# Kernel optimization log

Measured on AMD Instinct MI355X. Metric: run time of the kernel, lower is better.

## Reference

```python
import jax, jax.numpy as jnp
import numpy as np

B, T, E, H, DK, FF = 8, 2048, 64, 8, 8, 256
EPS = 1e-5


def _ln(x, g, b):
    m = jnp.mean(x, axis=-1, keepdims=True)
    v = jnp.mean((x - m) ** 2, axis=-1, keepdims=True)
    return (x - m) * jax.lax.rsqrt(v + EPS) * g + b


def setup_inputs() -> dict:
    key = jax.random.key(0)
    ks = jax.random.split(key, 16)
    s = 0.05
    f32 = jnp.float32
    return {
        "x": jax.random.normal(ks[0], (B, T, E), f32),
        "Wq": jax.random.normal(ks[1], (E, E), f32) * s,
        "bq": jnp.zeros((E,), f32),
        "Wk": jax.random.normal(ks[2], (E, E), f32) * s,
        "bk": jnp.zeros((E,), f32),
        "Wv": jax.random.normal(ks[3], (E, E), f32) * s,
        "bv": jnp.zeros((E,), f32),
        "Wo": jax.random.normal(ks[4], (E, E), f32) * s,
        "bo": jnp.zeros((E,), f32),
        "theta_attn": jax.random.uniform(ks[5], (), f32, 0.0, 2.0 * np.pi),
        "theta_ffn": jax.random.uniform(ks[6], (), f32, 0.0, 2.0 * np.pi),
        "W1": jax.random.normal(ks[7], (FF, E), f32) * s,
        "b1": jnp.zeros((FF,), f32),
        "W2": jax.random.normal(ks[8], (E, FF), f32) * s,
        "b2": jnp.zeros((E,), f32),
        "g1": jnp.ones((E,), f32),
        "be1": jnp.zeros((E,), f32),
        "g2": jnp.ones((E,), f32),
        "be2": jnp.zeros((E,), f32),
    }


def _forward(x, Wq, bq, Wk, bk, Wv, bv, Wo, bo, theta_attn, theta_ffn,
             W1, b1, W2, b2, g1, be1, g2, be2):
    def split(h):  # [B,T,E] -> [B,H,T,DK]
        return h.reshape(B, T, H, DK).transpose(0, 2, 1, 3)

    q = split(x @ Wq.T + bq)
    k = split(x @ Wk.T + bk)
    v = split(x @ Wv.T + bv)
    # per-head quantum circuit: RX(x) then shared RX(theta) -> <Z> = cos(x + theta)
    q = jnp.cos(q + theta_attn)
    k = jnp.cos(k + theta_attn)
    v = jnp.cos(v + theta_attn)
    scores = jnp.einsum('bhtd,bhsd->bhts', q, k) / np.float32(np.sqrt(DK))
    scores = jax.nn.softmax(scores, axis=-1)
    attn = jnp.einsum('bhts,bhsd->bhtd', scores, v)
    attn = attn.transpose(0, 2, 1, 3).reshape(B, T, E) @ Wo.T + bo
    x1 = _ln(x + attn, g1, be1)
    # FFN quantum circuit: RX(x) then shared RY(theta) -> <Z> = cos(x)*cos(theta)
    qout = jnp.cos(x1) * jnp.cos(theta_ffn)
    f = jax.nn.relu(qout @ W1.T + b1) @ W2.T + b2
    return _ln(x1 + f, g2, be2)


def reference(x, Wq, bq, Wk, bk, Wv, bv, Wo, bo, theta_attn, theta_ffn,
              W1, b1, W2, b2, g1, be1, g2, be2):
    return _forward(x, Wq, bq, Wk, bk, Wv, bv, Wo, bo, theta_attn, theta_ffn,
                    W1, b1, W2, b2, g1, be1, g2, be2)
```

## Files before the change

### kernel.cpp

```cpp
#include <hip/hip_runtime.h>
#include <hip/hip_bf16.h>

#define B_ 8
#define T_ 2048
#define NROWS 16384

typedef __attribute__((ext_vector_type(4))) float f32x4;
typedef __attribute__((ext_vector_type(16))) float f32x16;
typedef __attribute__((ext_vector_type(8))) short short8;
typedef __fp16 half2_t __attribute__((ext_vector_type(2)));

__device__ __forceinline__ unsigned short f2bf(float f) {
    __hip_bfloat16 h = __float2bfloat16(f);
    return *reinterpret_cast<unsigned short*>(&h);
}
__device__ __forceinline__ unsigned int pkrtz(float a, float b) {
    half2_t h = __builtin_amdgcn_cvt_pkrtz(a, b);
    return __builtin_bit_cast(unsigned int, h);
}
__device__ __forceinline__ float dot2(unsigned int a, unsigned int b, float c) {
    return __builtin_amdgcn_fdot2(__builtin_bit_cast(half2_t, a),
                                  __builtin_bit_cast(half2_t, b), c, false);
}
__device__ __forceinline__ float fast_exp2(float x) {
#if __has_builtin(__builtin_amdgcn_exp2f)
    return __builtin_amdgcn_exp2f(x);
#else
    return exp2f(x);
#endif
}

__global__ __launch_bounds__(512, 4) void qkv_kernel(
    const float* __restrict__ x,
    const float* __restrict__ Wq, const float* __restrict__ bq,
    const float* __restrict__ Wk, const float* __restrict__ bk,
    const float* __restrict__ Wv, const float* __restrict__ bv,
    const float* __restrict__ theta_attn,
    unsigned short* __restrict__ qb, unsigned short* __restrict__ kbuf,
    unsigned short* __restrict__ vbuf)
{
    __shared__ unsigned int xpk[32][34];
    __shared__ unsigned int wpk[32][196];
    const int tid = threadIdx.x;
    const int n0 = blockIdx.x * 32;

    {
        float4 v = ((const float4*)(x + (size_t)n0 * 64))[tid];
        int r = tid >> 4, k0 = (tid & 15) * 4;
        xpk[(k0 >> 1) + 0][r] = pkrtz(v.x, v.y);
        xpk[(k0 >> 1) + 1][r] = pkrtz(v.z, v.w);
    }
    const float* Wm[3] = {Wq, Wk, Wv};
    #pragma unroll
    for (int t = 0; t < 6; t++) {
        int fi = tid + t * 512;
        int m = fi >> 10, j = (fi >> 4) & 63, k0 = (fi & 15) * 4;
        float4 v = ((const float4*)Wm[m])[fi & 1023];
        wpk[(k0 >> 1) + 0][m * 64 + j] = pkrtz(v.x, v.y);
        wpk[(k0 >> 1) + 1][m * 64 + j] = pkrtz(v.z, v.w);
    }
    __syncthreads();

    const int r = tid >> 4;
    const int c0 = (tid & 15) * 12;
    float acc[12] = {};
    #pragma unroll 8
    for (int kp = 0; kp < 32; kp++) {
        unsigned int a = xpk[kp][r];
        uint4 b0 = *(const uint4*)&wpk[kp][c0];
        uint4 b1 = *(const uint4*)&wpk[kp][c0 + 4];
        uint4 b2 = *(const uint4*)&wpk[kp][c0 + 8];
        unsigned int bb[12] = {b0.x, b0.y, b0.z, b0.w,
                               b1.x, b1.y, b1.z, b1.w,
                               b2.x, b2.y, b2.z, b2.w};
        #pragma unroll
        for (int j = 0; j < 12; j++) acc[j] = dot2(a, bb[j], acc[j]);
    }

    const float th = *theta_attn;
    const float QS = 0.51006980f;
    const float* biasp[3] = {bq, bk, bv};
    unsigned short* outp3[3] = {qb, kbuf, vbuf};
    const int n = n0 + r;
    const int bI = n >> 11, tI = n & 2047;
    #pragma unroll
    for (int j = 0; j < 12; j++) {
        int c = c0 + j;
        int m = c >> 6, cc = c & 63;
        float val = __cosf(acc[j] + biasp[m][cc] + th);
        if (m == 0) val *= QS;
        size_t idx = ((size_t)(bI * 8 + (cc >> 3)) * 2048 + tI) * 8 + (cc & 7);
        outp3[m][idx] = f2bf(val);
    }
}

__global__ __launch_bounds__(256, 4) void attn_kernel(
    const unsigned short* __restrict__ qb,
    const unsigned short* __restrict__ kbuf,
    const unsigned short* __restrict__ vbuf,
    float* __restrict__ attn)
{
    __shared__ unsigned short Ks[1024 * 8];
    __shared__ unsigned short Vt[8 * 1032];
    const int tid = threadIdx.x;
    const int head = blockIdx.x >> 4;
    const int qblk = blockIdx.x & 15;
    const size_t hoff = (size_t)head * T_ * 8;
    const int wave = tid >> 6, lane = tid & 63;
    const int col = lane & 31, h = lane >> 5;
    const int q0 = qblk * 128 + wave * 32;

    const short8 z8 = {0, 0, 0, 0, 0, 0, 0, 0};
    short8 bqf = z8;
    if (h == 0) bqf = *(const short8*)(qb + hoff + (size_t)(q0 + col) * 8);

    f32x16 oacc = {0.f,0.f,0.f,0.f,0.f,0.f,0.f,0.f,0.f,0.f,0.f,0.f,0.f,0.f,0.f,0.f};
    const f32x16 z16 = {0.f,0.f,0.f,0.f,0.f,0.f,0.f,0.f,0.f,0.f,0.f,0.f,0.f,0.f,0.f,0.f};
    float lsum = 0.f;

    for (int half = 0; half < 2; half++) {
        __syncthreads();
        {
            const uint4* kg = (const uint4*)(kbuf + hoff + (size_t)half * 1024 * 8);
            const uint4* vg = (const uint4*)(vbuf + hoff + (size_t)half * 1024 * 8);
            uint4* kl = (uint4*)Ks;
            #pragma unroll
            for (int it = 0; it < 4; it++) {
                int s = tid + it * 256;
                kl[s] = kg[s];
                union { uint4 u; unsigned short us[8]; } cv;
                cv.u = vg[s];
                #pragma unroll
                for (int d = 0; d < 8; d++) Vt[d * 1032 + s] = cv.us[d];
            }
        }
        __syncthreads();

        for (int s0 = 0; s0 < 1024; s0 += 32) {
            short8 ak = z8;
            if (h == 0) ak = *(const short8*)&Ks[(s0 + col) * 8];
            f32x16 S = __builtin_amdgcn_mfma_f32_32x32x16_bf16(ak, bqf, z16, 0, 0, 0);
            float p[16];
            #pragma unroll
            for (int rr = 0; rr < 16; rr++) {
                p[rr] = fast_exp2(S[rr]);
                lsum += p[rr];
            }
            #pragma unroll
            for (int g = 0; g < 2; g++) {
                const float* pp = p + g * 8;
                unsigned int q01 = __builtin_amdgcn_perm(__float_as_uint(pp[1]), __float_as_uint(pp[0]), 0x07060302u);
                unsigned int q23 = __builtin_amdgcn_perm(__float_as_uint(pp[3]), __float_as_uint(pp[2]), 0x07060302u);
                unsigned int q45 = __builtin_amdgcn_perm(__float_as_uint(pp[5]), __float_as_uint(pp[4]), 0x07060302u);
                unsigned int q67 = __builtin_amdgcn_perm(__float_as_uint(pp[7]), __float_as_uint(pp[6]), 0x07060302u);
                unsigned int x01 = (unsigned int)__shfl_xor((int)q01, 32);
                unsigned int x23 = (unsigned int)__shfl_xor((int)q23, 32);
                unsigned int x45 = (unsigned int)__shfl_xor((int)q45, 32);
                unsigned int x67 = (unsigned int)__shfl_xor((int)q67, 32);
                union { unsigned int u[4]; short8 s; } bp;
                bp.u[0] = h ? x45 : q01;
                bp.u[1] = h ? x67 : q23;
                bp.u[2] = h ? q45 : x01;
                bp.u[3] = h ? q67 : x23;
                short8 av = z8;
                if (col < 8) av = *(const short8*)&Vt[col * 1032 + s0 + g * 16 + 8 * h];
                oacc = __builtin_amdgcn_mfma_f32_32x32x16_bf16(av, bp.s, oacc, 0, 0, 0);
            }
        }
    }

    lsum += __shfl_xor(lsum, 32);
    const float inv = 1.0f / lsum;
    const int bI = head >> 3, hI = head & 7;
    const int q = q0 + col;
    #pragma unroll
    for (int rr = 0; rr < 4; rr++) {
        int d = 4 * h + rr;
        attn[((size_t)bI * 2048 + q) * 64 + hI * 8 + d] = oacc[rr] * inv;
    }
}

__global__ __launch_bounds__(512, 4) void tail_kernel(
    const float* __restrict__ attn, const float* __restrict__ x,
    const float* __restrict__ Wo, const float* __restrict__ bo,
    const float* __restrict__ g1, const float* __restrict__ be1,
    const float* __restrict__ theta_ffn,
    const float* __restrict__ W1, const float* __restrict__ b1,
    const float* __restrict__ W2, const float* __restrict__ b2,
    const float* __restrict__ g2, const float* __restrict__ be2,
    float* __restrict__ outp)
{
    __shared__ unsigned int Wbuf[8704];
    __shared__ unsigned int qpk[32 * 66];
    __shared__ unsigned int Upk[128 * 66];
    const int tid = threadIdx.x;
    const int n0 = blockIdx.x * 64;
    const int r0 = (tid >> 4) * 2;
    const int c0 = (tid & 15) * 4;

    {
        const float4* ag = (const float4*)(attn + (size_t)n0 * 64);
        #pragma unroll
        for (int t = 0; t < 2; t++) {
            int fi = tid + t * 512;
            float4 v = ag[fi];
            int rr = fi >> 4, k0 = (fi & 15) * 4;
            Upk[((k0 >> 1) + 0) * 66 + rr] = pkrtz(v.x, v.y);
            Upk[((k0 >> 1) + 1) * 66 + rr] = pkrtz(v.z, v.w);
        }
        #pragma unroll
        for (int t = 0; t < 2; t++) {
            int fi = tid + t * 512;
            float4 v = ((const float4*)Wo)[fi];
            int nn = fi >> 4, k0 = (fi & 15) * 4;
            Wbuf[((k0 >> 1) + 0) * 68 + nn] = pkrtz(v.x, v.y);
            Wbuf[((k0 >> 1) + 1) * 68 + nn] = pkrtz(v.z, v.w);
        }
    }
    __syncthreads();

    float acc1[2][4] = {};
    #pragma unroll 8
    for (int kp = 0; kp < 32; kp++) {
        unsigned int a0 = Upk[kp * 66 + r0];
        unsigned int a1 = Upk[kp * 66 + r0 + 1];
        uint4 b = *(const uint4*)&Wbuf[kp * 68 + c0];
        unsigned int bb[4] = {b.x, b.y, b.z, b.w};
        #pragma unroll
        for (int j = 0; j < 4; j++) {
            acc1[0][j] = dot2(a0, bb[j], acc1[0][j]);
            acc1[1][j] = dot2(a1, bb[j], acc1[1][j]);
        }
    }

    float x1v[2][4];
    {
        float4 bo4 = *(const float4*)&bo[c0];
        float4 g14 = *(const float4*)&g1[c0];
        float4 be14 = *(const float4*)&be1[c0];
        float gg[4] = {g14.x, g14.y, g14.z, g14.w};
        float eb[4] = {be14.x, be14.y, be14.z, be14.w};
        float bb[4] = {bo4.x, bo4.y, bo4.z, bo4.w};
        float cth = __cosf(*theta_ffn);
        #pragma unroll
        for (int i = 0; i < 2; i++) {
            float4 xv = *(const float4*)(x + (size_t)(n0 + r0 + i) * 64 + c0);
            float vv[4] = {xv.x + acc1[i][0] + bb[0], xv.y + acc1[i][1] + bb[1],
                           xv.z + acc1[i][2] + bb[2], xv.w + acc1[i][3] + bb[3]};
            float s1 = vv[0] + vv[1] + vv[2] + vv[3];
            float s2 = vv[0]*vv[0] + vv[1]*vv[1] + vv[2]*vv[2] + vv[3]*vv[3];
            #pragma unroll
            for (int m = 1; m <= 8; m <<= 1) {
                s1 += __shfl_xor(s1, m, 16);
                s2 += __shfl_xor(s2, m, 16);
            }
            float mean = s1 * 0.015625f;
            float rstd = rsqrtf(s2 * 0.015625f - mean * mean + 1e-5f);
            float qv[4];
            #pragma unroll
            for (int j = 0; j < 4; j++) {
                x1v[i][j] = (vv[j] - mean) * rstd * gg[j] + eb[j];
                qv[j] = __cosf(x1v[i][j]) * cth;
            }
            qpk[((c0 >> 1) + 0) * 66 + r0 + i] = pkrtz(qv[0], qv[1]);
            qpk[((c0 >> 1) + 1) * 66 + r0 + i] = pkrtz(qv[2], qv[3]);
        }
    }
    __syncthreads();

    #pragma unroll
    for (int t = 0; t < 8; t++) {
        int fi = tid + t * 512;
        float4 v = ((const float4*)W1)[fi];
        int f = fi >> 4, k0 = (fi & 15) * 4;
        Wbuf[((k0 >> 1) + 0) * 260 + f] = pkrtz(v.x, v.y);
        Wbuf[((k0 >> 1) + 1) * 260 + f] = pkrtz(v.z, v.w);
    }
    __syncthreads();

    const int r2 = (tid >> 5) * 4;
    const int f0 = (tid & 31) * 8;
    float acc2[4][8] = {};
    #pragma unroll 4
    for (int kp = 0; kp < 32; kp++) {
        unsigned int a_[4];
        #pragma unroll
        for (int i = 0; i < 4; i++) a_[i] = qpk[kp * 66 + r2 + i];
        uint4 b0 = *(const uint4*)&Wbuf[kp * 260 + f0];
        uint4 b1_ = *(const uint4*)&Wbuf[kp * 260 + f0 + 4];
        unsigned int bb[8] = {b0.x, b0.y, b0.z, b0.w, b1_.x, b1_.y, b1_.z, b1_.w};
        #pragma unroll
        for (int i = 0; i < 4; i++)
            #pragma unroll
            for (int j = 0; j < 8; j++)
                acc2[i][j] = dot2(a_[i], bb[j], acc2[i][j]);
    }
    {
        float4 c1a = *(const float4*)&b1[f0];
        float4 c1b = *(const float4*)&b1[f0 + 4];
        float bb[8] = {c1a.x, c1a.y, c1a.z, c1a.w, c1b.x, c1b.y, c1b.z, c1b.w};
        #pragma unroll
        for (int i = 0; i < 4; i++) {
            float hv[8];
            #pragma unroll
            for (int j = 0; j < 8; j++) hv[j] = fmaxf(acc2[i][j] + bb[j], 0.f);
            #pragma unroll
            for (int jp = 0; jp < 4; jp++)
                Upk[(f0 / 2 + jp) * 66 + r2 + i] = pkrtz(hv[2 * jp], hv[2 * jp + 1]);
        }
    }
    __syncthreads();

    #pragma unroll
    for (int t = 0; t < 8; t++) {
        int fi = tid + t * 512;
        float4 v = ((const float4*)W2)[fi];
        int e = fi >> 6, k0 = (fi & 63) * 4;
        Wbuf[((k0 >> 1) + 0) * 68 + e] = pkrtz(v.x, v.y);
        Wbuf[((k0 >> 1) + 1) * 68 + e] = pkrtz(v.z, v.w);
    }
    __syncthreads();

    float acc3[2][4] = {};
    #pragma unroll 8
    for (int fp = 0; fp < 128; fp++) {
        unsigned int a0 = Upk[fp * 66 + r0];
        unsigned int a1 = Upk[fp * 66 + r0 + 1];
        uint4 b = *(const uint4*)&Wbuf[fp * 68 + c0];
        unsigned int bb[4] = {b.x, b.y, b.z, b.w};
        #pragma unroll
        for (int j = 0; j < 4; j++) {
            acc3[0][j] = dot2(a0, bb[j], acc3[0][j]);
            acc3[1][j] = dot2(a1, bb[j], acc3[1][j]);
        }
    }

    {
        float4 b24 = *(const float4*)&b2[c0];
        float4 g24 = *(const float4*)&g2[c0];
        float4 be24 = *(const float4*)&be2[c0];
        float bb[4] = {b24.x, b24.y, b24.z, b24.w};
        float gg[4] = {g24.x, g24.y, g24.z, g24.w};
        float eb[4] = {be24.x, be24.y, be24.z, be24.w};
        #pragma unroll
        for (int i = 0; i < 2; i++) {
            float vv[4];
            #pragma unroll
            for (int j = 0; j < 4; j++) vv[j] = x1v[i][j] + acc3[i][j] + bb[j];
            float s1 = vv[0] + vv[1] + vv[2] + vv[3];
            float s2 = vv[0]*vv[0] + vv[1]*vv[1] + vv[2]*vv[2] + vv[3]*vv[3];
            #pragma unroll
            for (int m = 1; m <= 8; m <<= 1) {
                s1 += __shfl_xor(s1, m, 16);
                s2 += __shfl_xor(s2, m, 16);
            }
            float mean = s1 * 0.015625f;
            float rstd = rsqrtf(s2 * 0.015625f - mean * mean + 1e-5f);
            float4 o;
            o.x = (vv[0] - mean) * rstd * gg[0] + eb[0];
            o.y = (vv[1] - mean) * rstd * gg[1] + eb[1];
            o.z = (vv[2] - mean) * rstd * gg[2] + eb[2];
            o.w = (vv[3] - mean) * rstd * gg[3] + eb[3];
            *(float4*)(outp + (size_t)(n0 + r0 + i) * 64 + c0) = o;
        }
    }
}

extern "C" void kernel_launch(void* const* d_in, const int* in_sizes, int n_in,
                              void* d_out, int out_size, void* d_ws, size_t ws_size,
                              hipStream_t stream)
{
    const float* x   = (const float*)d_in[0];
    const float* Wq  = (const float*)d_in[1];
    const float* bq  = (const float*)d_in[2];
    const float* Wk  = (const float*)d_in[3];
    const float* bk  = (const float*)d_in[4];
    const float* Wv  = (const float*)d_in[5];
    const float* bv  = (const float*)d_in[6];
    const float* Wo  = (const float*)d_in[7];
    const float* bo  = (const float*)d_in[8];
    const float* tha = (const float*)d_in[9];
    const float* thf = (const float*)d_in[10];
    const float* W1  = (const float*)d_in[11];
    const float* b1  = (const float*)d_in[12];
    const float* W2  = (const float*)d_in[13];
    const float* b2  = (const float*)d_in[14];
    const float* g1  = (const float*)d_in[15];
    const float* be1 = (const float*)d_in[16];
    const float* g2  = (const float*)d_in[17];
    const float* be2 = (const float*)d_in[18];

    char* wsb = (char*)d_ws;
    unsigned short* qbp = (unsigned short*)(wsb);
    unsigned short* kbp = (unsigned short*)(wsb + (2u << 20));
    unsigned short* vbp = (unsigned short*)(wsb + (4u << 20));
    float* attn = (float*)(wsb + (6u << 20));

    qkv_kernel<<<512, 512, 0, stream>>>(x, Wq, bq, Wk, bk, Wv, bv, tha, qbp, kbp, vbp);
    attn_kernel<<<1024, 256, 0, stream>>>(qbp, kbp, vbp, attn);
    tail_kernel<<<256, 512, 0, stream>>>(attn, x, Wo, bo, g1, be1, thf,
                                         W1, b1, W2, b2, g2, be2, (float*)d_out);
}
```

Before: 170.6 us.

## Stage QKV output through LDS for vector stores; halve tail tile and prefetch weights

```diff
diff --git a/kernel.cpp b/kernel.cpp
--- a/kernel.cpp
+++ b/kernel.cpp
@@ -41,6 +41,7 @@
 {
     __shared__ unsigned int xpk[32][34];
     __shared__ unsigned int wpk[32][196];
+    __shared__ unsigned short outs[32][216];
     const int tid = threadIdx.x;
     const int n0 = blockIdx.x * 32;
 
@@ -80,17 +81,36 @@
     const float th = *theta_attn;
     const float QS = 0.51006980f;
     const float* biasp[3] = {bq, bk, bv};
+    {
+        float vals[12];
+        #pragma unroll
+        for (int j = 0; j < 12; j++) {
+            int c = c0 + j;
+            int m = c >> 6, cc = c & 63;
+            float v = __cosf(acc[j] + biasp[m][cc] + th);
+            vals[j] = (m == 0) ? v * QS : v;
+        }
+        unsigned int* orow = (unsigned int*)&outs[r][c0];
+        #pragma unroll
+        for (int jp = 0; jp < 6; jp++)
+            orow[jp] = (unsigned int)f2bf(vals[2 * jp]) |
+                       ((unsigned int)f2bf(vals[2 * jp + 1]) << 16);
+    }
+    __syncthreads();
+
     unsigned short* outp3[3] = {qb, kbuf, vbuf};
-    const int n = n0 + r;
-    const int bI = n >> 11, tI = n & 2047;
-    #pragma unroll
-    for (int j = 0; j < 12; j++) {
-        int c = c0 + j;
-        int m = c >> 6, cc = c & 63;
-        float val = __cosf(acc[j] + biasp[m][cc] + th);
-        if (m == 0) val *= QS;
-        size_t idx = ((size_t)(bI * 8 + (cc >> 3)) * 2048 + tI) * 8 + (cc & 7);
-        outp3[m][idx] = f2bf(val);
+    #pragma unroll
+    for (int t = 0; t < 2; t++) {
+        int fi = tid + t * 512;
+        if (fi < 768) {
+            int m = fi >> 8, rest = fi & 255;
+            int hI = rest >> 5, r2 = rest & 31;
+            uint4 v = *(const uint4*)&outs[r2][m * 64 + hI * 8];
+            int n = n0 + r2;
+            unsigned short* dst = outp3[m] +
+                ((size_t)((n >> 11) * 8 + hI) * 2048 + (n & 2047)) * 8;
+            *(uint4*)dst = v;
+        }
     }
 }
 
@@ -190,123 +210,121 @@
     const float* __restrict__ g2, const float* __restrict__ be2,
     float* __restrict__ outp)
 {
-    __shared__ unsigned int Wbuf[8704];
-    __shared__ unsigned int qpk[32 * 66];
-    __shared__ unsigned int Upk[128 * 66];
+    __shared__ unsigned int Wbuf[10880];
+    __shared__ unsigned int qpk[32 * 34];
+    __shared__ unsigned int Upk[128 * 34];
     const int tid = threadIdx.x;
-    const int n0 = blockIdx.x * 64;
-    const int r0 = (tid >> 4) * 2;
+    const int n0 = blockIdx.x * 32;
+    const int r0 = tid >> 4;
     const int c0 = (tid & 15) * 4;
-
-    {
-        const float4* ag = (const float4*)(attn + (size_t)n0 * 64);
-        #pragma unroll
-        for (int t = 0; t < 2; t++) {
-            int fi = tid + t * 512;
-            float4 v = ag[fi];
-            int rr = fi >> 4, k0 = (fi & 15) * 4;
-            Upk[((k0 >> 1) + 0) * 66 + rr] = pkrtz(v.x, v.y);
-            Upk[((k0 >> 1) + 1) * 66 + rr] = pkrtz(v.z, v.w);
-        }
-        #pragma unroll
-        for (int t = 0; t < 2; t++) {
-            int fi = tid + t * 512;
-            float4 v = ((const float4*)Wo)[fi];
-            int nn = fi >> 4, k0 = (fi & 15) * 4;
-            Wbuf[((k0 >> 1) + 0) * 68 + nn] = pkrtz(v.x, v.y);
-            Wbuf[((k0 >> 1) + 1) * 68 + nn] = pkrtz(v.z, v.w);
-        }
-    }
-    __syncthreads();
-
-    float acc1[2][4] = {};
+    unsigned int* const W1p = Wbuf + 2176;
+    unsigned int* const W2p = Wbuf + 2176;
+
+    float4 atv = ((const float4*)(attn + (size_t)n0 * 64))[tid];
+    float4 wo0 = ((const float4*)Wo)[tid];
+    float4 wo1 = ((const float4*)Wo)[tid + 512];
+    float4 xv  = *(const float4*)(x + (size_t)(n0 + r0) * 64 + c0);
+    float4 w1r[8];
+    #pragma unroll
+    for (int t = 0; t < 8; t++) w1r[t] = ((const float4*)W1)[tid + t * 512];
+
+    {
+        int rr = tid >> 4, k0 = (tid & 15) * 4;
+        Upk[((k0 >> 1) + 0) * 34 + rr] = pkrtz(atv.x, atv.y);
+        Upk[((k0 >> 1) + 1) * 34 + rr] = pkrtz(atv.z, atv.w);
+    }
+    {
+        int nn = tid >> 4, k0 = (tid & 15) * 4;
+        Wbuf[((k0 >> 1) + 0) * 68 + nn] = pkrtz(wo0.x, wo0.y);
+        Wbuf[((k0 >> 1) + 1) * 68 + nn] = pkrtz(wo0.z, wo0.w);
+        int fi = tid + 512;
+        nn = fi >> 4; k0 = (fi & 15) * 4;
+        Wbuf[((k0 >> 1) + 0) * 68 + nn] = pkrtz(wo1.x, wo1.y);
+        Wbuf[((k0 >> 1) + 1) * 68 + nn] = pkrtz(wo1.z, wo1.w);
+    }
+    __syncthreads();
+
+    #pragma unroll
+    for (int t = 0; t < 8; t++) {
+        int fi = tid + t * 512;
+        int f = fi >> 4, k0 = (fi & 15) * 4;
+        W1p[((k0 >> 1) + 0) * 260 + f] = pkrtz(w1r[t].x, w1r[t].y);
+        W1p[((k0 >> 1) + 1) * 260 + f] = pkrtz(w1r[t].z, w1r[t].w);
+    }
+
+    float acc1[4] = {};
     #pragma unroll 8
     for (int kp = 0; kp < 32; kp++) {
-        unsigned int a0 = Upk[kp * 66 + r0];
-        unsigned int a1 = Upk[kp * 66 + r0 + 1];
+        unsigned int a = Upk[kp * 34 + r0];
         uint4 b = *(const uint4*)&Wbuf[kp * 68 + c0];
-        unsigned int bb[4] = {b.x, b.y, b.z, b.w};
-        #pragma unroll
-        for (int j = 0; j < 4; j++) {
-            acc1[0][j] = dot2(a0, bb[j], acc1[0][j]);
-            acc1[1][j] = dot2(a1, bb[j], acc1[1][j]);
-        }
-    }
-
-    float x1v[2][4];
+        acc1[0] = dot2(a, b.x, acc1[0]);
+        acc1[1] = dot2(a, b.y, acc1[1]);
+        acc1[2] = dot2(a, b.z, acc1[2]);
+        acc1[3] = dot2(a, b.w, acc1[3]);
+    }
+
+    float x1v[4];
     {
         float4 bo4 = *(const float4*)&bo[c0];
         float4 g14 = *(const float4*)&g1[c0];
         float4 be14 = *(const float4*)&be1[c0];
+        float cth = __cosf(*theta_ffn);
+        float vv[4] = {xv.x + acc1[0] + bo4.x, xv.y + acc1[1] + bo4.y,
+                       xv.z + acc1[2] + bo4.z, xv.w + acc1[3] + bo4.w};
+        float s1 = vv[0] + vv[1] + vv[2] + vv[3];
+        float s2 = vv[0]*vv[0] + vv[1]*vv[1] + vv[2]*vv[2] + vv[3]*vv[3];
+        #pragma unroll
+        for (int m = 1; m <= 8; m <<= 1) {
+            s1 += __shfl_xor(s1, m, 16);
+            s2 += __shfl_xor(s2, m, 16);
+        }
+        float mean = s1 * 0.015625f;
+        float rstd = rsqrtf(s2 * 0.015625f - mean * mean + 1e-5f);
         float gg[4] = {g14.x, g14.y, g14.z, g14.w};
         float eb[4] = {be14.x, be14.y, be14.z, be14.w};
-        float bb[4] = {bo4.x, bo4.y, bo4.z, bo4.w};
-        float cth = __cosf(*theta_ffn);
-        #pragma unroll
-        for (int i = 0; i < 2; i++) {
-            float4 xv = *(const float4*)(x + (size_t)(n0 + r0 + i) * 64 + c0);
-            float vv[4] = {xv.x + acc1[i][0] + bb[0], xv.y + acc1[i][1] + bb[1],
-                           xv.z + acc1[i][2] + bb[2], xv.w + acc1[i][3] + bb[3]};
-            float s1 = vv[0] + vv[1] + vv[2] + vv[3];
-            float s2 = vv[0]*vv[0] + vv[1]*vv[1] + vv[2]*vv[2] + vv[3]*vv[3];
-            #pragma unroll
-            for (int m = 1; m <= 8; m <<= 1) {
-                s1 += __shfl_xor(s1, m, 16);
-                s2 += __shfl_xor(s2, m, 16);
-            }
-            float mean = s1 * 0.015625f;
-            float rstd = rsqrtf(s2 * 0.015625f - mean * mean + 1e-5f);
-            float qv[4];
-            #pragma unroll
-            for (int j = 0; j < 4; j++) {
-                x1v[i][j] = (vv[j] - mean) * rstd * gg[j] + eb[j];
-                qv[j] = __cosf(x1v[i][j]) * cth;
-            }
-            qpk[((c0 >> 1) + 0) * 66 + r0 + i] = pkrtz(qv[0], qv[1]);
-            qpk[((c0 >> 1) + 1) * 66 + r0 + i] = pkrtz(qv[2], qv[3]);
-        }
-    }
-    __syncthreads();
-
-    #pragma unroll
-    for (int t = 0; t < 8; t++) {
-        int fi = tid + t * 512;
-        float4 v = ((const float4*)W1)[fi];
-        int f = fi >> 4, k0 = (fi & 15) * 4;
-        Wbuf[((k0 >> 1) + 0) * 260 + f] = pkrtz(v.x, v.y);
-        Wbuf[((k0 >> 1) + 1) * 260 + f] = pkrtz(v.z, v.w);
-    }
-    __syncthreads();
-
-    const int r2 = (tid >> 5) * 4;
+        float qv[4];
+        #pragma unroll
+        for (int j = 0; j < 4; j++) {
+            x1v[j] = (vv[j] - mean) * rstd * gg[j] + eb[j];
+            qv[j] = __cosf(x1v[j]) * cth;
+        }
+        qpk[((c0 >> 1) + 0) * 34 + r0] = pkrtz(qv[0], qv[1]);
+        qpk[((c0 >> 1) + 1) * 34 + r0] = pkrtz(qv[2], qv[3]);
+    }
+    __syncthreads();
+
+    float4 w2r[8];
+    #pragma unroll
+    for (int t = 0; t < 8; t++) w2r[t] = ((const float4*)W2)[tid + t * 512];
+
+    const int r2 = (tid >> 5) * 2;
     const int f0 = (tid & 31) * 8;
-    float acc2[4][8] = {};
+    float acc2[2][8] = {};
     #pragma unroll 4
     for (int kp = 0; kp < 32; kp++) {
-        unsigned int a_[4];
-        #pragma unroll
-        for (int i = 0; i < 4; i++) a_[i] = qpk[kp * 66 + r2 + i];
-        uint4 b0 = *(const uint4*)&Wbuf[kp * 260 + f0];
-        uint4 b1_ = *(const uint4*)&Wbuf[kp * 260 + f0 + 4];
+        unsigned int a0 = qpk[kp * 34 + r2];
+        unsigned int a1 = qpk[kp * 34 + r2 + 1];
+        uint4 b0 = *(const uint4*)&W1p[kp * 260 + f0];
+        uint4 b1_ = *(const uint4*)&W1p[kp * 260 + f0 + 4];
         unsigned int bb[8] = {b0.x, b0.y, b0.z, b0.w, b1_.x, b1_.y, b1_.z, b1_.w};
         #pragma unroll
-        for (int i = 0; i < 4; i++)
-            #pragma unroll
-            for (int j = 0; j < 8; j++)
-                acc2[i][j] = dot2(a_[i], bb[j], acc2[i][j]);
+        for (int j = 0; j < 8; j++) {
+            acc2[0][j] = dot2(a0, bb[j], acc2[0][j]);
+            acc2[1][j] = dot2(a1, bb[j], acc2[1][j]);
+        }
     }
     {
         float4 c1a = *(const float4*)&b1[f0];
         float4 c1b = *(const float4*)&b1[f0 + 4];
         float bb[8] = {c1a.x, c1a.y, c1a.z, c1a.w, c1b.x, c1b.y, c1b.z, c1b.w};
         #pragma unroll
-        for (int i = 0; i < 4; i++) {
+        for (int i = 0; i < 2; i++) {
             float hv[8];
             #pragma unroll
             for (int j = 0; j < 8; j++) hv[j] = fmaxf(acc2[i][j] + bb[j], 0.f);
             #pragma unroll
             for (int jp = 0; jp < 4; jp++)
-                Upk[(f0 / 2 + jp) * 66 + r2 + i] = pkrtz(hv[2 * jp], hv[2 * jp + 1]);
+                Upk[(f0 / 2 + jp) * 34 + r2 + i] = pkrtz(hv[2 * jp], hv[2 * jp + 1]);
         }
     }
     __syncthreads();
@@ -314,55 +332,44 @@
     #pragma unroll
     for (int t = 0; t < 8; t++) {
         int fi = tid + t * 512;
-        float4 v = ((const float4*)W2)[fi];
         int e = fi >> 6, k0 = (fi & 63) * 4;
-        Wbuf[((k0 >> 1) + 0) * 68 + e] = pkrtz(v.x, v.y);
-        Wbuf[((k0 >> 1) + 1) * 68 + e] = pkrtz(v.z, v.w);
-    }
-    __syncthreads();
-
-    float acc3[2][4] = {};
+        W2p[((k0 >> 1) + 0) * 68 + e] = pkrtz(w2r[t].x, w2r[t].y);
+        W2p[((k0 >> 1) + 1) * 68 + e] = pkrtz(w2r[t].z, w2r[t].w);
+    }
+    __syncthreads();
+
+    float acc3[4] = {};
     #pragma unroll 8
     for (int fp = 0; fp < 128; fp++) {
-        unsigned int a0 = Upk[fp * 66 + r0];
-        unsigned int a1 = Upk[fp * 66 + r0 + 1];
-        uint4 b = *(const uint4*)&Wbuf[fp * 68 + c0];
-        unsigned int bb[4] = {b.x, b.y, b.z, b.w};
-        #pragma unroll
-        for (int j = 0; j < 4; j++) {
-            acc3[0][j] = dot2(a0, bb[j], acc3[0][j]);
-            acc3[1][j] = dot2(a1, bb[j], acc3[1][j]);
-        }
+        unsigned int a = Upk[fp * 34 + r0];
+        uint4 b = *(const uint4*)&W2p[fp * 68 + c0];
+        acc3[0] = dot2(a, b.x, acc3[0]);
+        acc3[1] = dot2(a, b.y, acc3[1]);
+        acc3[2] = dot2(a, b.z, acc3[2]);
+        acc3[3] = dot2(a, b.w, acc3[3]);
     }
 
     {
         float4 b24 = *(const float4*)&b2[c0];
         float4 g24 = *(const float4*)&g2[c0];
         float4 be24 = *(const float4*)&be2[c0];
-        float bb[4] = {b24.x, b24.y, b24.z, b24.w};
-        float gg[4] = {g24.x, g24.y, g24.z, g24.w};
-        float eb[4] = {be24.x, be24.y, be24.z, be24.w};
-        #pragma unroll
-        for (int i = 0; i < 2; i++) {
-            float vv[4];
-            #pragma unroll
-            for (int j = 0; j < 4; j++) vv[j] = x1v[i][j] + acc3[i][j] + bb[j];
-            float s1 = vv[0] + vv[1] + vv[2] + vv[3];
-            float s2 = vv[0]*vv[0] + vv[1]*vv[1] + vv[2]*vv[2] + vv[3]*vv[3];
-            #pragma unroll
-            for (int m = 1; m <= 8; m <<= 1) {
-                s1 += __shfl_xor(s1, m, 16);
-                s2 += __shfl_xor(s2, m, 16);
-            }
-            float mean = s1 * 0.015625f;
-            float rstd = rsqrtf(s2 * 0.015625f - mean * mean + 1e-5f);
-            float4 o;
-            o.x = (vv[0] - mean) * rstd * gg[0] + eb[0];
-            o.y = (vv[1] - mean) * rstd * gg[1] + eb[1];
-            o.z = (vv[2] - mean) * rstd * gg[2] + eb[2];
-            o.w = (vv[3] - mean) * rstd * gg[3] + eb[3];
-            *(float4*)(outp + (size_t)(n0 + r0 + i) * 64 + c0) = o;
-        }
+        float vv[4] = {x1v[0] + acc3[0] + b24.x, x1v[1] + acc3[1] + b24.y,
+                       x1v[2] + acc3[2] + b24.z, x1v[3] + acc3[3] + b24.w};
+        float s1 = vv[0] + vv[1] + vv[2] + vv[3];
+        float s2 = vv[0]*vv[0] + vv[1]*vv[1] + vv[2]*vv[2] + vv[3]*vv[3];
+        #pragma unroll
+        for (int m = 1; m <= 8; m <<= 1) {
+            s1 += __shfl_xor(s1, m, 16);
+            s2 += __shfl_xor(s2, m, 16);
+        }
+        float mean = s1 * 0.015625f;
+        float rstd = rsqrtf(s2 * 0.015625f - mean * mean + 1e-5f);
+        float4 o;
+        o.x = (vv[0] - mean) * rstd * g24.x + be24.x;
+        o.y = (vv[1] - mean) * rstd * g24.y + be24.y;
+        o.z = (vv[2] - mean) * rstd * g24.z + be24.z;
+        o.w = (vv[3] - mean) * rstd * g24.w + be24.w;
+        *(float4*)(outp + (size_t)(n0 + r0) * 64 + c0) = o;
     }
 }
 
@@ -398,6 +405,6 @@
 
     qkv_kernel<<<512, 512, 0, stream>>>(x, Wq, bq, Wk, bk, Wv, bv, tha, qbp, kbp, vbp);
     attn_kernel<<<1024, 256, 0, stream>>>(qbp, kbp, vbp, attn);
-    tail_kernel<<<256, 512, 0, stream>>>(attn, x, Wo, bo, g1, be1, thf,
+    tail_kernel<<<512, 512, 0, stream>>>(attn, x, Wo, bo, g1, be1, thf,
                                          W1, b1, W2, b2, g2, be2, (float*)d_out);
 }
```

Result: faster. 165.4 us (-3.0%).
